# Kernel optimization log

Hardware: AMD Instinct MI355X
Metric: run time of the kernel (lower is better)

## Reference

```python
import jax, jax.numpy as jnp
import numpy as np

N_GROUPS = 4


def setup_inputs() -> dict:
    key = jax.random.key(0)
    ks = jax.random.split(key, 6)
    I, J, B = 512, 512, 4  # query tokens, key tokens, grid batch (B = 1 * n_groups)
    n_dim, out_per_group = 128, 4  # n_heads // n_groups = 16 // 4
    grid_q = jax.random.normal(ks[0], (I, 3), dtype=jnp.float32)
    grid_kv = jax.random.normal(ks[1], (B, J, 3), dtype=jnp.float32)
    W1 = jax.random.normal(ks[2], (3, n_dim), dtype=jnp.float32) * (1.0 / np.sqrt(3))
    b1 = jnp.zeros((n_dim,), dtype=jnp.float32)
    W2 = jax.random.normal(ks[3], (n_dim, n_dim), dtype=jnp.float32) * (1.0 / np.sqrt(n_dim))
    b2 = jnp.zeros((n_dim,), dtype=jnp.float32)
    W3 = jax.random.normal(ks[4], (n_dim, out_per_group), dtype=jnp.float32) * (1.0 / np.sqrt(n_dim))
    b3 = jnp.zeros((out_per_group,), dtype=jnp.float32)
    return {"grid_q": grid_q, "grid_kv": grid_kv, "W1": W1, "b1": b1,
            "W2": W2, "b2": b2, "W3": W3, "b3": b3}


def reference(grid_q, grid_kv, W1, b1, W2, b2, W3, b3):
    # grid_q: [I, 3] -> [1, I, 3]; grid_kv: [B, J, 3]
    gq = grid_q[None, :, :]
    # pairwise position difference: [B, I, J, 3]
    pos = gq[:, :, None, :] - grid_kv[:, None, :, :]
    # sign-log transform
    bias = jnp.sign(pos) * jnp.log1p(jnp.abs(pos))
    # tiny MLP: 3 -> n_dim -> n_dim -> heads//groups, pointwise over (B, I, J)
    h = jax.nn.relu(jnp.einsum('bijc,cd->bijd', bias, W1) + b1)
    h = jax.nn.relu(jnp.einsum('bijd,de->bije', h, W2) + b2)
    out = jnp.einsum('bije,eo->bijo', h, W3) + b3  # [B, I, J, O]
    # rearrange '(b g) i j o -> b (g o) i j' with g = N_GROUPS
    B, I, J, O = out.shape
    out = out.reshape(B // N_GROUPS, N_GROUPS, I, J, O)
    out = jnp.transpose(out, (0, 1, 4, 2, 3)).reshape(B // N_GROUPS, N_GROUPS * O, I, J)
    return out
```

## Files before the change

kernel.cpp:

```cpp
#include <hip/hip_runtime.h>
#include <math.h>

#define NBLOCKS 2048
#define THREADS 256
#define TILE 64
#define POS_PER_BLOCK 512
#define ITERS 8
#define CH 512

typedef __attribute__((ext_vector_type(8)))  short  short8;
typedef __attribute__((ext_vector_type(4)))  float  float4v;
typedef __attribute__((ext_vector_type(4)))  unsigned uint4v;
typedef __attribute__((ext_vector_type(16))) float  float16;

__device__ __forceinline__ unsigned cvt_pk(float lo, float hi) {
    unsigned r;
    asm("v_cvt_pk_bf16_f32 %0, %1, %2" : "=v"(r) : "v"(lo), "v"(hi));
    return r;
}


__device__ __forceinline__ int kmap(int c, int jj) {
    return 32 * (c >> 2) + 16 * ((c >> 1) & 1) + 4 * (c & 1) + ((jj >> 2) << 3) + (jj & 3);
}

__global__ __launch_bounds__(256, 3)
void crpb_mfma8(const float* __restrict__ gq,
                const float* __restrict__ gkv,
                const float* __restrict__ W1,
                const float* __restrict__ b1,
                const float* __restrict__ W2,
                const float* __restrict__ b2,
                const float* __restrict__ W3,
                const float* __restrict__ b3,
                float* __restrict__ out)
{
    __shared__ __align__(16) unsigned short ash[2][16 * CH];
    __shared__ __align__(16) float red[2][2 * 4 * 64];
    __shared__ __align__(16) float b2s[128];
    __shared__ __align__(16) unsigned fA[512][4];
    __shared__ __align__(16) unsigned fB[512];

    const int tid  = threadIdx.x;
    const int lane = tid & 63;
    const int w    = __builtin_amdgcn_readfirstlane(tid >> 6);
    const int l31  = lane & 31;
    const int lh   = lane >> 5;

    if (tid < 128) b2s[tid] = b2[tid];

    const int ct2 = w & 1;
    const int ph  = w >> 1;
    const int pofs = ph * 32 + l31;

    float16 z16;
    #pragma unroll
    for (int r = 0; r < 16; ++r) z16[r] = 0.0f;

    short8 w1f[2];
    #pragma unroll
    for (int mt = 0; mt < 2; ++mt) {
        const int ch = (ct2 * 2 + mt) * 32 + l31;
        const float w0 = W1[ch], w1v = W1[128 + ch], w2v = W1[256 + ch], b1v = b1[ch];
        const float w0h = __uint_as_float(cvt_pk(w0, w0) << 16);
        const float w1h = __uint_as_float(cvt_pk(w1v, w1v) << 16);
        const float w2h = __uint_as_float(cvt_pk(w2v, w2v) << 16);
        const float b1h = __uint_as_float(cvt_pk(b1v, b1v) << 16);
        const float w0l = w0 - w0h, w1l = w1v - w1h, w2l = w2v - w2h, b1l = b1v - b1h;
        unsigned d[4];
        if (lh == 0) {
            d[0] = cvt_pk(w0h, w0l);
            d[1] = cvt_pk(w0h, w1h);
            d[2] = cvt_pk(w1l, w1h);
            d[3] = cvt_pk(w2h, w2l);
        } else {
            d[0] = cvt_pk(w2h, b1h);
            d[1] = cvt_pk(b1l, 0.0f);
            d[2] = 0; d[3] = 0;
        }
        __builtin_memcpy(&w1f[mt], d, 16);
    }

    short8 a2f[2][8];
    #pragma unroll
    for (int mt = 0; mt < 2; ++mt) {
        const int e = ct2 * 64 + mt * 32 + l31;
        #pragma unroll
        for (int ks = 0; ks < 8; ++ks) {
            const int c = 2 * ks + lh;
            unsigned t0[4];
            #pragma unroll
            for (int t = 0; t < 4; ++t) {
                const int d0 = kmap(c, 2 * t), d1 = d0 + 1;
                t0[t] = cvt_pk(W2[d0 * 128 + e], W2[d1 * 128 + e]);
            }
            __builtin_memcpy(&a2f[mt][ks], t0, 16);
        }
    }

    short8 w3a[2][2];
    #pragma unroll
    for (int mt = 0; mt < 2; ++mt) {
        #pragma unroll
        for (int m2 = 0; m2 < 2; ++m2) {
            unsigned tt[4];
            #pragma unroll
            for (int t = 0; t < 4; ++t) {
                const int chl = ((2 * t) & 3) + 8 * ((2 * t) >> 2) + 4 * lh + 16 * m2;
                const int ch0 = (ct2 * 2 + mt) * 32 + chl, ch1 = ch0 + 1;
                const float lo = (l31 < 4) ? W3[ch0 * 4 + l31] : 0.0f;
                const float hi = (l31 < 4) ? W3[ch1 * 4 + l31] : 0.0f;
                tt[t] = cvt_pk(lo, hi);
            }
            __builtin_memcpy(&w3a[mt][m2], tt, 16);
        }
    }
    const float b3r = b3[w];

    const int posblock = blockIdx.x * POS_PER_BLOCK;
    const int bb = posblock >> 18;
    const int i  = (posblock >> 9) & 511;
    const float q0 = gq[i * 3 + 0], q1 = gq[i * 3 + 1], q2 = gq[i * 3 + 2];
    const float* kvrow = gkv + (size_t)(bb << 9) * 3;

    for (int jj = tid; jj < 512; jj += THREADS) {
        const float k0 = kvrow[jj * 3 + 0], k1 = kvrow[jj * 3 + 1], k2 = kvrow[jj * 3 + 2];
        const float c0 = q0 - k0, c1 = q1 - k1, c2 = q2 - k2;
        const float f0 = copysignf(__logf(1.0f + fabsf(c0)), c0);
        const float f1 = copysignf(__logf(1.0f + fabsf(c1)), c1);
        const float f2 = copysignf(__logf(1.0f + fabsf(c2)), c2);
        const unsigned u0 = cvt_pk(f0, f0), u2 = cvt_pk(f2, f2);
        const float f0h = __uint_as_float(u0 << 16);
        const float f1h = __uint_as_float(cvt_pk(f1, f1) << 16);
        const float f2h = __uint_as_float(u2 << 16);
        const float f0l = f0 - f0h, f1l = f1 - f1h, f2l = f2 - f2h;
        fA[jj][0] = u0;
        fA[jj][1] = cvt_pk(f0l, f1);
        fA[jj][2] = cvt_pk(f1, f1l);
        fA[jj][3] = u2;
        fB[jj]    = cvt_pk(f2l, 1.0f);
    }
    __syncthreads();

    auto phaseA = [&](int x, int buf) {
        const int jpos = x * TILE + pofs;
        unsigned d[4];
        if (lh == 0) {
            const uint4v t = *(const uint4v*)&fA[jpos][0];
            d[0] = t[0]; d[1] = t[1]; d[2] = t[2]; d[3] = t[3];
        } else {
            d[0] = fB[jpos];
            d[1] = 0x00003F80u;
            d[2] = 0; d[3] = 0;
        }
        short8 bf; __builtin_memcpy(&bf, d, 16);

        #pragma unroll
        for (int mt = 0; mt < 2; ++mt) {
            const int cti = ct2 * 2 + mt;
            float16 c1r = __builtin_amdgcn_mfma_f32_32x32x16_bf16(w1f[mt], bf, z16, 0, 0, 0);
            unsigned pk0[4], pk1[4];
            #pragma unroll
            for (int t = 0; t < 4; ++t) {
                pk0[t] = cvt_pk(fmaxf(c1r[2 * t], 0.f),     fmaxf(c1r[2 * t + 1], 0.f));
                pk1[t] = cvt_pk(fmaxf(c1r[8 + 2 * t], 0.f), fmaxf(c1r[8 + 2 * t + 1], 0.f));
            }
            short8 v0, v1;
            __builtin_memcpy(&v0, pk0, 16);
            __builtin_memcpy(&v1, pk1, 16);
            *(short8*)&ash[buf][(4 * cti + lh) * CH + pofs * 8]     = v0;
            *(short8*)&ash[buf][(4 * cti + 2 + lh) * CH + pofs * 8] = v1;
        }
    };

    phaseA(0, 0);
    __syncthreads();

    for (int it = 0; it < ITERS; ++it) {
        const int buf = it & 1;
        const int jb = it * TILE;

        float16 acc0, acc1;
        #pragma unroll
        for (int qr = 0; qr < 4; ++qr) {
            float4v i0 = *(const float4v*)&b2s[(ct2 * 2 + 0) * 32 + 8 * qr + 4 * lh];
            float4v i1 = *(const float4v*)&b2s[(ct2 * 2 + 1) * 32 + 8 * qr + 4 * lh];
            #pragma unroll
            for (int t = 0; t < 4; ++t) { acc0[4 * qr + t] = i0[t]; acc1[4 * qr + t] = i1[t]; }
        }
        const unsigned short* br = &ash[buf][lh * CH + pofs * 8];

        __builtin_amdgcn_s_setprio(1);
        #pragma unroll
        for (int ks = 0; ks < 8; ++ks) {
            short8 bfrag = *(const short8*)(br + ks * 2 * CH);
            acc0 = __builtin_amdgcn_mfma_f32_32x32x16_bf16(a2f[0][ks], bfrag, acc0, 0, 0, 0);
            acc1 = __builtin_amdgcn_mfma_f32_32x32x16_bf16(a2f[1][ks], bfrag, acc1, 0, 0, 0);
        }

        {
            unsigned pa0[4], pa1[4], pb0[4], pb1[4];
            #pragma unroll
            for (int t = 0; t < 4; ++t) {
                pa0[t] = cvt_pk(fmaxf(acc0[2 * t], 0.f),     fmaxf(acc0[2 * t + 1], 0.f));
                pa1[t] = cvt_pk(fmaxf(acc0[8 + 2 * t], 0.f), fmaxf(acc0[8 + 2 * t + 1], 0.f));
                pb0[t] = cvt_pk(fmaxf(acc1[2 * t], 0.f),     fmaxf(acc1[2 * t + 1], 0.f));
                pb1[t] = cvt_pk(fmaxf(acc1[8 + 2 * t], 0.f), fmaxf(acc1[8 + 2 * t + 1], 0.f));
            }
            short8 fa0, fa1, fb0, fb1;
            __builtin_memcpy(&fa0, pa0, 16); __builtin_memcpy(&fa1, pa1, 16);
            __builtin_memcpy(&fb0, pb0, 16); __builtin_memcpy(&fb1, pb1, 16);
            float16 p;
            p = __builtin_amdgcn_mfma_f32_32x32x16_bf16(w3a[0][0], fa0, z16, 0, 0, 0);
            p = __builtin_amdgcn_mfma_f32_32x32x16_bf16(w3a[0][1], fa1, p, 0, 0, 0);
            p = __builtin_amdgcn_mfma_f32_32x32x16_bf16(w3a[1][0], fb0, p, 0, 0, 0);
            p = __builtin_amdgcn_mfma_f32_32x32x16_bf16(w3a[1][1], fb1, p, 0, 0, 0);
            __builtin_amdgcn_s_setprio(0);
            if (lh == 0) {
                #pragma unroll
                for (int o = 0; o < 4; ++o)
                    red[buf][ct2 * 256 + o * 64 + pofs] = p[o];
            }
        }

        if (it != ITERS - 1) phaseA(it + 1, 1 - buf);

        __syncthreads();

        {
            const int o = w, pos = lane;
            const float v = b3r + red[buf][o * 64 + pos] + red[buf][256 + o * 64 + pos];
            out[((size_t)((bb << 2) + o) << 18) + ((size_t)i << 9) + jb + pos] = v;
        }
    }
}

extern "C" void kernel_launch(void* const* d_in, const int* in_sizes, int n_in,
                              void* d_out, int out_size, void* d_ws, size_t ws_size,
                              hipStream_t stream) {
    const float* gq  = (const float*)d_in[0];
    const float* gkv = (const float*)d_in[1];
    const float* W1  = (const float*)d_in[2];
    const float* b1  = (const float*)d_in[3];
    const float* W2  = (const float*)d_in[4];
    const float* b2  = (const float*)d_in[5];
    const float* W3  = (const float*)d_in[6];
    const float* b3  = (const float*)d_in[7];
    float* out = (float*)d_out;

    crpb_mfma8<<<NBLOCKS, THREADS, 0, stream>>>(gq, gkv, W1, b1, W2, b2, W3, b3, out);
}
```

Measured before the change: 122.7 us.

## Split hidden channels across 8 waves instead of 4 per block

```diff
diff --git a/kernel.cpp b/kernel.cpp
--- a/kernel.cpp
+++ b/kernel.cpp
@@ -2,7 +2,7 @@
 #include <math.h>
 
 #define NBLOCKS 2048
-#define THREADS 256
+#define THREADS 512
 #define TILE 64
 #define POS_PER_BLOCK 512
 #define ITERS 8
@@ -24,7 +24,7 @@
     return 32 * (c >> 2) + 16 * ((c >> 1) & 1) + 4 * (c & 1) + ((jj >> 2) << 3) + (jj & 3);
 }
 
-__global__ __launch_bounds__(256, 3)
+__global__ __launch_bounds__(512, 4)
 void crpb_mfma8(const float* __restrict__ gq,
                 const float* __restrict__ gkv,
                 const float* __restrict__ W1,
@@ -36,7 +36,7 @@
                 float* __restrict__ out)
 {
     __shared__ __align__(16) unsigned short ash[2][16 * CH];
-    __shared__ __align__(16) float red[2][2 * 4 * 64];
+    __shared__ __align__(16) float red[2][4 * 4 * 64];
     __shared__ __align__(16) float b2s[128];
     __shared__ __align__(16) unsigned fA[512][4];
     __shared__ __align__(16) unsigned fB[512];
@@ -49,18 +49,17 @@
 
     if (tid < 128) b2s[tid] = b2[tid];
 
-    const int ct2 = w & 1;
-    const int ph  = w >> 1;
+    const int ct = w & 3;
+    const int ph = w >> 2;
     const int pofs = ph * 32 + l31;
 
     float16 z16;
     #pragma unroll
     for (int r = 0; r < 16; ++r) z16[r] = 0.0f;
 
-    short8 w1f[2];
-    #pragma unroll
-    for (int mt = 0; mt < 2; ++mt) {
-        const int ch = (ct2 * 2 + mt) * 32 + l31;
+    short8 w1f;
+    {
+        const int ch = ct * 32 + l31;
         const float w0 = W1[ch], w1v = W1[128 + ch], w2v = W1[256 + ch], b1v = b1[ch];
         const float w0h = __uint_as_float(cvt_pk(w0, w0) << 16);
         const float w1h = __uint_as_float(cvt_pk(w1v, w1v) << 16);
@@ -78,13 +77,12 @@
             d[1] = cvt_pk(b1l, 0.0f);
             d[2] = 0; d[3] = 0;
         }
-        __builtin_memcpy(&w1f[mt], d, 16);
-    }
-
-    short8 a2f[2][8];
-    #pragma unroll
-    for (int mt = 0; mt < 2; ++mt) {
-        const int e = ct2 * 64 + mt * 32 + l31;
+        __builtin_memcpy(&w1f, d, 16);
+    }
+
+    short8 a2f[8];
+    {
+        const int e = ct * 32 + l31;
         #pragma unroll
         for (int ks = 0; ks < 8; ++ks) {
             const int c = 2 * ks + lh;
@@ -94,28 +92,25 @@
                 const int d0 = kmap(c, 2 * t), d1 = d0 + 1;
                 t0[t] = cvt_pk(W2[d0 * 128 + e], W2[d1 * 128 + e]);
             }
-            __builtin_memcpy(&a2f[mt][ks], t0, 16);
-        }
-    }
-
-    short8 w3a[2][2];
+            __builtin_memcpy(&a2f[ks], t0, 16);
+        }
+    }
+
+    short8 w3a[2];
     #pragma unroll
-    for (int mt = 0; mt < 2; ++mt) {
-        #pragma unroll
-        for (int m2 = 0; m2 < 2; ++m2) {
-            unsigned tt[4];
-            #pragma unroll
-            for (int t = 0; t < 4; ++t) {
-                const int chl = ((2 * t) & 3) + 8 * ((2 * t) >> 2) + 4 * lh + 16 * m2;
-                const int ch0 = (ct2 * 2 + mt) * 32 + chl, ch1 = ch0 + 1;
-                const float lo = (l31 < 4) ? W3[ch0 * 4 + l31] : 0.0f;
-                const float hi = (l31 < 4) ? W3[ch1 * 4 + l31] : 0.0f;
-                tt[t] = cvt_pk(lo, hi);
-            }
-            __builtin_memcpy(&w3a[mt][m2], tt, 16);
-        }
-    }
-    const float b3r = b3[w];
+    for (int m2 = 0; m2 < 2; ++m2) {
+        unsigned tt[4];
+        #pragma unroll
+        for (int t = 0; t < 4; ++t) {
+            const int chl = ((2 * t) & 3) + 8 * ((2 * t) >> 2) + 4 * lh + 16 * m2;
+            const int ch0 = ct * 32 + chl, ch1 = ch0 + 1;
+            const float lo = (l31 < 4) ? W3[ch0 * 4 + l31] : 0.0f;
+            const float hi = (l31 < 4) ? W3[ch1 * 4 + l31] : 0.0f;
+            tt[t] = cvt_pk(lo, hi);
+        }
+        __builtin_memcpy(&w3a[m2], tt, 16);
+    }
+    const float b3r = b3[w & 3];
 
     const int posblock = blockIdx.x * POS_PER_BLOCK;
     const int bb = posblock >> 18;
@@ -155,22 +150,18 @@
         }
         short8 bf; __builtin_memcpy(&bf, d, 16);
 
-        #pragma unroll
-        for (int mt = 0; mt < 2; ++mt) {
-            const int cti = ct2 * 2 + mt;
-            float16 c1r = __builtin_amdgcn_mfma_f32_32x32x16_bf16(w1f[mt], bf, z16, 0, 0, 0);
-            unsigned pk0[4], pk1[4];
-            #pragma unroll
-            for (int t = 0; t < 4; ++t) {
-                pk0[t] = cvt_pk(fmaxf(c1r[2 * t], 0.f),     fmaxf(c1r[2 * t + 1], 0.f));
-                pk1[t] = cvt_pk(fmaxf(c1r[8 + 2 * t], 0.f), fmaxf(c1r[8 + 2 * t + 1], 0.f));
-            }
-            short8 v0, v1;
-            __builtin_memcpy(&v0, pk0, 16);
-            __builtin_memcpy(&v1, pk1, 16);
-            *(short8*)&ash[buf][(4 * cti + lh) * CH + pofs * 8]     = v0;
-            *(short8*)&ash[buf][(4 * cti + 2 + lh) * CH + pofs * 8] = v1;
-        }
+        float16 c1r = __builtin_amdgcn_mfma_f32_32x32x16_bf16(w1f, bf, z16, 0, 0, 0);
+        unsigned pk0[4], pk1[4];
+        #pragma unroll
+        for (int t = 0; t < 4; ++t) {
+            pk0[t] = cvt_pk(fmaxf(c1r[2 * t], 0.f),     fmaxf(c1r[2 * t + 1], 0.f));
+            pk1[t] = cvt_pk(fmaxf(c1r[8 + 2 * t], 0.f), fmaxf(c1r[8 + 2 * t + 1], 0.f));
+        }
+        short8 v0, v1;
+        __builtin_memcpy(&v0, pk0, 16);
+        __builtin_memcpy(&v1, pk1, 16);
+        *(short8*)&ash[buf][(4 * ct + lh) * CH + pofs * 8]     = v0;
+        *(short8*)&ash[buf][(4 * ct + 2 + lh) * CH + pofs * 8] = v1;
     };
 
     phaseA(0, 0);
@@ -180,13 +171,12 @@
         const int buf = it & 1;
         const int jb = it * TILE;
 
-        float16 acc0, acc1;
+        float16 acc;
         #pragma unroll
         for (int qr = 0; qr < 4; ++qr) {
-            float4v i0 = *(const float4v*)&b2s[(ct2 * 2 + 0) * 32 + 8 * qr + 4 * lh];
-            float4v i1 = *(const float4v*)&b2s[(ct2 * 2 + 1) * 32 + 8 * qr + 4 * lh];
+            float4v i0 = *(const float4v*)&b2s[ct * 32 + 8 * qr + 4 * lh];
             #pragma unroll
-            for (int t = 0; t < 4; ++t) { acc0[4 * qr + t] = i0[t]; acc1[4 * qr + t] = i1[t]; }
+            for (int t = 0; t < 4; ++t) acc[4 * qr + t] = i0[t];
         }
         const unsigned short* br = &ash[buf][lh * CH + pofs * 8];
 
@@ -194,32 +184,26 @@
         #pragma unroll
         for (int ks = 0; ks < 8; ++ks) {
             short8 bfrag = *(const short8*)(br + ks * 2 * CH);
-            acc0 = __builtin_amdgcn_mfma_f32_32x32x16_bf16(a2f[0][ks], bfrag, acc0, 0, 0, 0);
-            acc1 = __builtin_amdgcn_mfma_f32_32x32x16_bf16(a2f[1][ks], bfrag, acc1, 0, 0, 0);
+            acc = __builtin_amdgcn_mfma_f32_32x32x16_bf16(a2f[ks], bfrag, acc, 0, 0, 0);
         }
 
         {
-            unsigned pa0[4], pa1[4], pb0[4], pb1[4];
+            unsigned pa0[4], pa1[4];
             #pragma unroll
             for (int t = 0; t < 4; ++t) {
-                pa0[t] = cvt_pk(fmaxf(acc0[2 * t], 0.f),     fmaxf(acc0[2 * t + 1], 0.f));
-                pa1[t] = cvt_pk(fmaxf(acc0[8 + 2 * t], 0.f), fmaxf(acc0[8 + 2 * t + 1], 0.f));
-                pb0[t] = cvt_pk(fmaxf(acc1[2 * t], 0.f),     fmaxf(acc1[2 * t + 1], 0.f));
-                pb1[t] = cvt_pk(fmaxf(acc1[8 + 2 * t], 0.f), fmaxf(acc1[8 + 2 * t + 1], 0.f));
+                pa0[t] = cvt_pk(fmaxf(acc[2 * t], 0.f),     fmaxf(acc[2 * t + 1], 0.f));
+                pa1[t] = cvt_pk(fmaxf(acc[8 + 2 * t], 0.f), fmaxf(acc[8 + 2 * t + 1], 0.f));
             }
-            short8 fa0, fa1, fb0, fb1;
+            short8 fa0, fa1;
             __builtin_memcpy(&fa0, pa0, 16); __builtin_memcpy(&fa1, pa1, 16);
-            __builtin_memcpy(&fb0, pb0, 16); __builtin_memcpy(&fb1, pb1, 16);
             float16 p;
-            p = __builtin_amdgcn_mfma_f32_32x32x16_bf16(w3a[0][0], fa0, z16, 0, 0, 0);
-            p = __builtin_amdgcn_mfma_f32_32x32x16_bf16(w3a[0][1], fa1, p, 0, 0, 0);
-            p = __builtin_amdgcn_mfma_f32_32x32x16_bf16(w3a[1][0], fb0, p, 0, 0, 0);
-            p = __builtin_amdgcn_mfma_f32_32x32x16_bf16(w3a[1][1], fb1, p, 0, 0, 0);
+            p = __builtin_amdgcn_mfma_f32_32x32x16_bf16(w3a[0], fa0, z16, 0, 0, 0);
+            p = __builtin_amdgcn_mfma_f32_32x32x16_bf16(w3a[1], fa1, p, 0, 0, 0);
             __builtin_amdgcn_s_setprio(0);
             if (lh == 0) {
                 #pragma unroll
                 for (int o = 0; o < 4; ++o)
-                    red[buf][ct2 * 256 + o * 64 + pofs] = p[o];
+                    red[buf][ct * 256 + o * 64 + pofs] = p[o];
             }
         }
 
@@ -227,9 +211,13 @@
 
         __syncthreads();
 
-        {
+        if (w < 4) {
             const int o = w, pos = lane;
-            const float v = b3r + red[buf][o * 64 + pos] + red[buf][256 + o * 64 + pos];
+            const float v = b3r
+                          + red[buf][0 * 256 + o * 64 + pos]
+                          + red[buf][1 * 256 + o * 64 + pos]
+                          + red[buf][2 * 256 + o * 64 + pos]
+                          + red[buf][3 * 256 + o * 64 + pos];
             out[((size_t)((bb << 2) + o) << 18) + ((size_t)i << 9) + jb + pos] = v;
         }
     }
```

Measured after the change: 118.9 us. 3.2% less time.
